# Kernel tuning notes

Hardware: AMD Instinct MI355X
Metric: run time of the kernel (lower is better)

The kernel has to match this reference:

```python
import jax, jax.numpy as jnp
import numpy as np

N, H, NDIM = 512, 64, 32  # batch, channels, SPD matrix side


def setup_inputs() -> dict:
    key = jax.random.key(0)
    A = jax.random.normal(key, (N, H, NDIM, NDIM), dtype=jnp.float32) * 0.5
    # well-conditioned SPD inputs: A A^T / n + I
    X = jnp.einsum('bhij,bhkj->bhik', A, A) / NDIM + jnp.eye(NDIM, dtype=jnp.float32)
    s = jnp.asarray(1.0, dtype=jnp.float32)  # learnable scalar scale
    return {"X": X, "s": s}


def reference(X, s):
    # Log-Cholesky SPD batch norm (training mode): Frechet mean/var under the
    # Log-Cholesky metric, center to identity, rescale geodesically by s/sqrt(var).
    Nb, h, n, _ = X.shape
    Xf = X.reshape(Nb * h, n, n)                      # (M, n, n)
    L = jnp.linalg.cholesky(Xf)                        # lower Cholesky factors
    sl = jnp.tril(L, -1)                               # strictly lower part
    d = jnp.diagonal(L, axis1=-2, axis2=-1)            # (M, n) positive diagonals
    logd = jnp.log(d)

    # Frechet mean in Log-Cholesky coordinates
    sl_mean = sl.mean(axis=0)                          # (n, n) strictly lower
    logd_mean = logd.mean(axis=0)                      # (n,)

    # variance = mean squared Log-Cholesky distance to the mean
    sl_c = sl - sl_mean                                # centered strictly-lower coords
    logd_c = logd - logd_mean                          # centered log-diagonal coords
    dist2 = (sl_c ** 2).sum(axis=(-2, -1)) + (logd_c ** 2).sum(axis=-1)
    var = dist2.mean()

    # center + geodesic scaling by factor = s / sqrt(var)
    factor = s / jnp.sqrt(var)
    eye = jnp.eye(n, dtype=X.dtype)
    L_out = factor * sl_c + jnp.exp(factor * logd_c)[:, :, None] * eye  # (M, n, n)
    X_out = jnp.einsum('mij,mkj->mik', L_out, L_out)   # L L^T back to SPD
    return X_out.reshape(Nb, h, n, n)
```

## Files before the change

### kernel.cpp

```cpp
#include <hip/hip_runtime.h>
#include <cmath>

#define NM 32768
#define ND 32
#define NSLICE 16
#define SLICE_STRIDE 1088
#define FMBASE (NSLICE * SLICE_STRIDE)

typedef __attribute__((ext_vector_type(8))) short short8;
typedef __attribute__((ext_vector_type(16))) float f32x16;

template<int L>
__device__ __forceinline__ float bcast32(float x) {
    return __int_as_float(__builtin_amdgcn_ds_swizzle(__float_as_int(x), (L << 5)));
}

template<int J, int L>
__device__ __forceinline__ void rank1_upd(float (&a)[ND], float lrj) {
    if constexpr (L < ND) {
        float blj = bcast32<L>(lrj);
        a[L] = fmaf(-lrj, blj, a[L]);
        rank1_upd<J, L + 1>(a, lrj);
    }
}

template<int J>
__device__ __forceinline__ void chol_steps(float (&a)[ND], int r) {
    if constexpr (J < ND) {
        float ajj = bcast32<J>(a[J]);
        float rs = __builtin_amdgcn_rsqf(ajj);
        float lrj = ((r == J) ? ajj : a[J]) * rs;
        a[J] = lrj;
        rank1_upd<J, J + 1>(a, lrj);
        chol_steps<J + 1>(a, r);
    }
}

union frag_u { short8 v; int i[4]; };

__device__ __forceinline__ void build_frags(const frag_u& mine_lo, const frag_u& mine_hi,
                                            bool hi_half, frag_u& f0, frag_u& f1) {
    #pragma unroll
    for (int w = 0; w < 4; ++w) {
        int olo = __shfl_xor(mine_lo.i[w], 32);
        int ohi = __shfl_xor(mine_hi.i[w], 32);
        f0.i[w] = hi_half ? ohi : mine_lo.i[w];
        f1.i[w] = hi_half ? mine_hi.i[w] : olo;
    }
}


__global__ __launch_bounds__(256, 4) void k1_stats(const float* __restrict__ X,
                                                   float* __restrict__ gacc,
                                                   float* __restrict__ Lbuf) {
    __shared__ float lacc[1057];
    int tid = threadIdx.x;
    for (int i = tid; i < 1057; i += 256) lacc[i] = 0.0f;
    __syncthreads();

    int lane = tid & 63;
    int r = lane & 31;
    int wave = tid >> 6;

    for (int pass = 0; pass < 2; ++pass) {
        int mp = (blockIdx.x * 2 + pass) * 4 + wave;
        int mat = mp * 2 + (lane >> 5);
        const float* xm = X + (size_t)mat * (ND * ND);

        float a[ND];
        #pragma unroll
        for (int j = 0; j < ND; ++j) a[j] = xm[j * ND + r];

        chol_steps<0>(a, r);

        float* lm = Lbuf + (size_t)mat * (ND * ND);
        #pragma unroll
        for (int j = 0; j < ND; ++j) lm[j * ND + r] = a[j];

        float diag = a[0];
        #pragma unroll
        for (int j = 1; j < ND; ++j) diag = (r == j) ? a[j] : diag;
        float logd = logf(diag);

        float sq = logd * logd;
        #pragma unroll
        for (int j = 0; j < ND; ++j) if (j < r) sq = fmaf(a[j], a[j], sq);
        #pragma unroll
        for (int k = 1; k < 64; k <<= 1) sq += __shfl_xor(sq, k);
        if (lane == 0) atomicAdd(&lacc[1056], sq);

        #pragma unroll
        for (int j = 0; j < ND; ++j) if (j < r) atomicAdd(&lacc[j * ND + r], a[j]);
        atomicAdd(&lacc[1024 + r], logd);
    }

    __syncthreads();
    float* g = gacc + (size_t)(blockIdx.x & (NSLICE - 1)) * SLICE_STRIDE;
    for (int i = tid; i < 1057; i += 256) atomicAdd(&g[i], lacc[i]);
}

__global__ __launch_bounds__(256) void k2_final(const float* __restrict__ sscal,
                                                float* __restrict__ ws) {
    __shared__ float red[256];
    __shared__ float s2sh;
    __shared__ float sfactor;
    int tid = threadIdx.x;
    const float invM = 1.0f / (float)NM;

    float msq = 0.0f;
    for (int k = tid; k < 1057; k += 256) {
        float s = 0.0f;
        #pragma unroll
        for (int sl = 0; sl < NSLICE; ++sl) s += ws[sl * SLICE_STRIDE + k];
        if (k < 1056) {
            float m = s * invM;
            ws[FMBASE + k] = m;
            msq = fmaf(m, m, msq);
        } else {
            s2sh = s;
        }
    }
    red[tid] = msq;
    __syncthreads();
    for (int s = 128; s > 0; s >>= 1) {
        if (tid < s) red[tid] += red[tid + s];
        __syncthreads();
    }
    if (tid == 0) {
        float var = s2sh * invM - red[0];
        float f = sscal[0] / sqrtf(var);
        sfactor = f;
        ws[FMBASE + 1056] = f;
    }
    __syncthreads();
    float f = sfactor;
    for (int k = tid; k < 1056; k += 256) ws[FMBASE + k] *= f;
}

__global__ __launch_bounds__(256, 4) void k3_out(const float* __restrict__ wsf,
                                                 float* __restrict__ out) {
    int tid = threadIdx.x;
    int lane = tid & 63;
    int r = lane & 31;
    int wave = tid >> 6;
    int pair = blockIdx.x * 4 + wave;
    int mat = pair * 2 + (lane >> 5);
    bool hi_half = (lane >> 5) != 0;

    const float* lm = out + (size_t)mat * (ND * ND);
    float a[ND];
    #pragma unroll
    for (int j = 0; j < ND; ++j) a[j] = lm[j * ND + r];
    float diag = lm[r * ND + r];

    float factor = wsf[1056];
    float dval = expf(fmaf(factor, logf(diag), -wsf[1024 + r]));

    f32x16 acc0, acc1;
    #pragma unroll
    for (int g = 0; g < 16; ++g) { acc0[g] = 0.0f; acc1[g] = 0.0f; }

    #pragma unroll
    for (int kb = 0; kb < 32; kb += 16) {
        frag_u mlo_h, mhi_h, mlo_l, mhi_l;
        #pragma unroll
        for (int i = 0; i < 8; ++i) {
            int j0 = kb + i, j1 = kb + 8 + i;
            float t0 = fmaf(factor, a[j0], -wsf[j0 * ND + r]);
            float v0 = (j0 < r) ? t0 : ((j0 == r) ? dval : 0.0f);
            float t1 = fmaf(factor, a[j1], -wsf[j1 * ND + r]);
            float v1 = (j1 < r) ? t1 : ((j1 == r) ? dval : 0.0f);
            __bf16 hb0 = (__bf16)v0, hb1 = (__bf16)v1;
            mlo_h.v[i] = __builtin_bit_cast(short, hb0);
            mhi_h.v[i] = __builtin_bit_cast(short, hb1);
            mlo_l.v[i] = __builtin_bit_cast(short, (__bf16)(v0 - (float)hb0));
            mhi_l.v[i] = __builtin_bit_cast(short, (__bf16)(v1 - (float)hb1));
        }
        frag_u h0, h1, l0, l1;
        build_frags(mlo_h, mhi_h, hi_half, h0, h1);
        build_frags(mlo_l, mhi_l, hi_half, l0, l1);
        acc0 = __builtin_amdgcn_mfma_f32_32x32x16_bf16(h0.v, h0.v, acc0, 0, 0, 0);
        acc1 = __builtin_amdgcn_mfma_f32_32x32x16_bf16(h1.v, h1.v, acc1, 0, 0, 0);
        acc0 = __builtin_amdgcn_mfma_f32_32x32x16_bf16(h0.v, l0.v, acc0, 0, 0, 0);
        acc1 = __builtin_amdgcn_mfma_f32_32x32x16_bf16(h1.v, l1.v, acc1, 0, 0, 0);
        acc0 = __builtin_amdgcn_mfma_f32_32x32x16_bf16(l0.v, h0.v, acc0, 0, 0, 0);
        acc1 = __builtin_amdgcn_mfma_f32_32x32x16_bf16(l1.v, h1.v, acc1, 0, 0, 0);
    }

    float* om0 = out + (size_t)(pair * 2) * (ND * ND);
    float* om1 = om0 + ND * ND;
    int col = lane & 31;
    int rb = (lane >> 5) * 4;
    #pragma unroll
    for (int g = 0; g < 16; ++g) {
        int row = (g & 3) + 8 * (g >> 2) + rb;
        om0[row * ND + col] = acc0[g];
        om1[row * ND + col] = acc1[g];
    }
}

extern "C" void kernel_launch(void* const* d_in, const int* in_sizes, int n_in,
                              void* d_out, int out_size, void* d_ws, size_t ws_size,
                              hipStream_t stream) {
    const float* X = (const float*)d_in[0];
    const float* s = (const float*)d_in[1];
    float* out = (float*)d_out;
    float* ws = (float*)d_ws;

    hipMemsetAsync(ws, 0, NSLICE * SLICE_STRIDE * sizeof(float), stream);
    hipLaunchKernelGGL(k1_stats, dim3(2048), dim3(256), 0, stream, X, ws, out);
    hipLaunchKernelGGL(k2_final, dim3(1), dim3(256), 0, stream, s, ws);
    hipLaunchKernelGGL(k3_out, dim3(4096), dim3(256), 0, stream, ws + FMBASE, out);
}
```

Measured before the change: 347.4 us.

## Restructure Cholesky step, hoist MFMA fragment packing, raise occupancy, fewer slices

The Cholesky inner step now scales the column by a reciprocal of the broadcast pivot and applies the rank-1 update before normalizing, so each step's sqrt and update no longer depend on each other. In k3, all MFMA fragments are built before any MFMA is issued, giving the scheduler more independent work to overlap. Both main kernels raise their launch-bounds occupancy hint from 4 to 6, and the global accumulation slices drop from 16 to 4. The risks are register spills from the tighter hint, more atomic contention on fewer slices, and small numeric differences from the reordered Cholesky arithmetic.

Measured after the change: 369.7 us. 1.06x slower.

```diff
diff --git a/kernel.cpp b/kernel.cpp
--- a/kernel.cpp
+++ b/kernel.cpp
@@ -3,7 +3,7 @@
 
 #define NM 32768
 #define ND 32
-#define NSLICE 16
+#define NSLICE 4
 #define SLICE_STRIDE 1088
 #define FMBASE (NSLICE * SLICE_STRIDE)
 
@@ -16,22 +16,23 @@
 }
 
 template<int J, int L>
-__device__ __forceinline__ void rank1_upd(float (&a)[ND], float lrj) {
+__device__ __forceinline__ void rank1_new(float (&a)[ND], float t) {
     if constexpr (L < ND) {
-        float blj = bcast32<L>(lrj);
-        a[L] = fmaf(-lrj, blj, a[L]);
-        rank1_upd<J, L + 1>(a, lrj);
+        float bLJ = bcast32<L>(a[J]);
+        a[L] = fmaf(-t, bLJ, a[L]);
+        rank1_new<J, L + 1>(a, t);
     }
 }
 
 template<int J>
 __device__ __forceinline__ void chol_steps(float (&a)[ND], int r) {
     if constexpr (J < ND) {
-        float ajj = bcast32<J>(a[J]);
-        float rs = __builtin_amdgcn_rsqf(ajj);
-        float lrj = ((r == J) ? ajj : a[J]) * rs;
-        a[J] = lrj;
-        rank1_upd<J, J + 1>(a, lrj);
+        float bJJ = bcast32<J>(a[J]);
+        float inv = __builtin_amdgcn_rcpf(bJJ);
+        float rs  = __builtin_amdgcn_rsqf(bJJ);
+        float t = a[J] * inv;
+        rank1_new<J, J + 1>(a, t);
+        a[J] *= rs;
         chol_steps<J + 1>(a, r);
     }
 }
@@ -49,8 +50,31 @@
     }
 }
 
-
-__global__ __launch_bounds__(256, 4) void k1_stats(const float* __restrict__ X,
+template<int KB>
+__device__ __forceinline__ void pack_quad(const float (&a)[ND], int r, float dval,
+                                          float factor, const float* __restrict__ wsf,
+                                          bool hi_half,
+                                          frag_u& h0, frag_u& h1, frag_u& l0, frag_u& l1) {
+    frag_u mlo_h, mhi_h, mlo_l, mhi_l;
+    #pragma unroll
+    for (int i = 0; i < 8; ++i) {
+        int j0 = KB + i, j1 = KB + 8 + i;
+        float t0 = fmaf(factor, a[j0], -wsf[j0 * ND + r]);
+        float v0 = (j0 < r) ? t0 : ((j0 == r) ? dval : 0.0f);
+        float t1 = fmaf(factor, a[j1], -wsf[j1 * ND + r]);
+        float v1 = (j1 < r) ? t1 : ((j1 == r) ? dval : 0.0f);
+        __bf16 hb0 = (__bf16)v0, hb1 = (__bf16)v1;
+        mlo_h.v[i] = __builtin_bit_cast(short, hb0);
+        mhi_h.v[i] = __builtin_bit_cast(short, hb1);
+        mlo_l.v[i] = __builtin_bit_cast(short, (__bf16)(v0 - (float)hb0));
+        mhi_l.v[i] = __builtin_bit_cast(short, (__bf16)(v1 - (float)hb1));
+    }
+    build_frags(mlo_h, mhi_h, hi_half, h0, h1);
+    build_frags(mlo_l, mhi_l, hi_half, l0, l1);
+}
+
+
+__global__ __launch_bounds__(256, 6) void k1_stats(const float* __restrict__ X,
                                                    float* __restrict__ gacc,
                                                    float* __restrict__ Lbuf) {
     __shared__ float lacc[1057];
@@ -137,7 +161,7 @@
     for (int k = tid; k < 1056; k += 256) ws[FMBASE + k] *= f;
 }
 
-__global__ __launch_bounds__(256, 4) void k3_out(const float* __restrict__ wsf,
+__global__ __launch_bounds__(256, 6) void k3_out(const float* __restrict__ wsf,
                                                  float* __restrict__ out) {
     int tid = threadIdx.x;
     int lane = tid & 63;
@@ -156,36 +180,26 @@
     float factor = wsf[1056];
     float dval = expf(fmaf(factor, logf(diag), -wsf[1024 + r]));
 
+    frag_u h0a, h1a, l0a, l1a, h0b, h1b, l0b, l1b;
+    pack_quad<0>(a, r, dval, factor, wsf, hi_half, h0a, h1a, l0a, l1a);
+    pack_quad<16>(a, r, dval, factor, wsf, hi_half, h0b, h1b, l0b, l1b);
+
     f32x16 acc0, acc1;
     #pragma unroll
     for (int g = 0; g < 16; ++g) { acc0[g] = 0.0f; acc1[g] = 0.0f; }
 
-    #pragma unroll
-    for (int kb = 0; kb < 32; kb += 16) {
-        frag_u mlo_h, mhi_h, mlo_l, mhi_l;
-        #pragma unroll
-        for (int i = 0; i < 8; ++i) {
-            int j0 = kb + i, j1 = kb + 8 + i;
-            float t0 = fmaf(factor, a[j0], -wsf[j0 * ND + r]);
-            float v0 = (j0 < r) ? t0 : ((j0 == r) ? dval : 0.0f);
-            float t1 = fmaf(factor, a[j1], -wsf[j1 * ND + r]);
-            float v1 = (j1 < r) ? t1 : ((j1 == r) ? dval : 0.0f);
-            __bf16 hb0 = (__bf16)v0, hb1 = (__bf16)v1;
-            mlo_h.v[i] = __builtin_bit_cast(short, hb0);
-            mhi_h.v[i] = __builtin_bit_cast(short, hb1);
-            mlo_l.v[i] = __builtin_bit_cast(short, (__bf16)(v0 - (float)hb0));
-            mhi_l.v[i] = __builtin_bit_cast(short, (__bf16)(v1 - (float)hb1));
-        }
-        frag_u h0, h1, l0, l1;
-        build_frags(mlo_h, mhi_h, hi_half, h0, h1);
-        build_frags(mlo_l, mhi_l, hi_half, l0, l1);
-        acc0 = __builtin_amdgcn_mfma_f32_32x32x16_bf16(h0.v, h0.v, acc0, 0, 0, 0);
-        acc1 = __builtin_amdgcn_mfma_f32_32x32x16_bf16(h1.v, h1.v, acc1, 0, 0, 0);
-        acc0 = __builtin_amdgcn_mfma_f32_32x32x16_bf16(h0.v, l0.v, acc0, 0, 0, 0);
-        acc1 = __builtin_amdgcn_mfma_f32_32x32x16_bf16(h1.v, l1.v, acc1, 0, 0, 0);
-        acc0 = __builtin_amdgcn_mfma_f32_32x32x16_bf16(l0.v, h0.v, acc0, 0, 0, 0);
-        acc1 = __builtin_amdgcn_mfma_f32_32x32x16_bf16(l1.v, h1.v, acc1, 0, 0, 0);
-    }
+    acc0 = __builtin_amdgcn_mfma_f32_32x32x16_bf16(h0a.v, h0a.v, acc0, 0, 0, 0);
+    acc1 = __builtin_amdgcn_mfma_f32_32x32x16_bf16(h1a.v, h1a.v, acc1, 0, 0, 0);
+    acc0 = __builtin_amdgcn_mfma_f32_32x32x16_bf16(h0a.v, l0a.v, acc0, 0, 0, 0);
+    acc1 = __builtin_amdgcn_mfma_f32_32x32x16_bf16(h1a.v, l1a.v, acc1, 0, 0, 0);
+    acc0 = __builtin_amdgcn_mfma_f32_32x32x16_bf16(l0a.v, h0a.v, acc0, 0, 0, 0);
+    acc1 = __builtin_amdgcn_mfma_f32_32x32x16_bf16(l1a.v, h1a.v, acc1, 0, 0, 0);
+    acc0 = __builtin_amdgcn_mfma_f32_32x32x16_bf16(h0b.v, h0b.v, acc0, 0, 0, 0);
+    acc1 = __builtin_amdgcn_mfma_f32_32x32x16_bf16(h1b.v, h1b.v, acc1, 0, 0, 0);
+    acc0 = __builtin_amdgcn_mfma_f32_32x32x16_bf16(h0b.v, l0b.v, acc0, 0, 0, 0);
+    acc1 = __builtin_amdgcn_mfma_f32_32x32x16_bf16(h1b.v, l1b.v, acc1, 0, 0, 0);
+    acc0 = __builtin_amdgcn_mfma_f32_32x32x16_bf16(l0b.v, h0b.v, acc0, 0, 0, 0);
+    acc1 = __builtin_amdgcn_mfma_f32_32x32x16_bf16(l1b.v, h1b.v, acc1, 0, 0, 0);
 
     float* om0 = out + (size_t)(pair * 2) * (ND * ND);
     float* om1 = om0 + ND * ND;
```
